# Kernel optimization log

Measured on AMD Instinct MI355X. Metric: run time of the kernel, lower is better.

Reference implementation:

```python
import jax, jax.numpy as jnp
import numpy as np

WS, OWS, NHEAD = 4, 6, 6          # window, overlap window = 4 + int(0.5*4), heads
B, CIN, COU, H, W = 2, 192, 192, 224, 224
MID = CIN  # r = 1


def calc_rpi_oca(ws=WS, ows=OWS):
    # relative position index between ws x ws query window and ows x ows overlapping kv window
    co = np.stack(np.meshgrid(np.arange(ws), np.arange(ws), indexing='ij')).reshape(2, -1)
    ce = np.stack(np.meshgrid(np.arange(ows), np.arange(ows), indexing='ij')).reshape(2, -1)
    rel = (ce[:, None, :] - co[:, :, None]).transpose(1, 2, 0) + (ws - 1)  # [ws*ws, ows*ows, 2], >= 0
    idx = rel[..., 0] * (ws + ows - 1) + rel[..., 1]                       # in [0, (ws+ows-1)^2)
    return jnp.asarray(idx)  # [16, 36]

RPI = calc_rpi_oca()


def conv2d(x, w, b, pad):
    out = jax.lax.conv_general_dilated(x, w, (1, 1), [(pad, pad), (pad, pad)],
                                       dimension_numbers=('NCHW', 'OIHW', 'NCHW'))
    return out + b[None, :, None, None]


def group_norm(x, g, b, groups, eps=1e-5):
    n = x.shape[0]
    xg = x.reshape(n, groups, -1)
    mu = xg.mean(-1, keepdims=True)
    var = xg.var(-1, keepdims=True)
    xn = ((xg - mu) * jax.lax.rsqrt(var + eps)).reshape(x.shape)
    return xn * g[None, :, None, None] + b[None, :, None, None]


def layer_norm(x, g, b, eps=1e-5):
    mu = x.mean(-1, keepdims=True)
    var = x.var(-1, keepdims=True)
    return (x - mu) * jax.lax.rsqrt(var + eps) * g + b


def ocab(x, h, w, ln1_g, ln1_b, qkv_w, qkv_b, rpb, proj_w, proj_b,
         ln2_g, ln2_b, fc1_w, fc1_b, fc2_w, fc2_b):
    b, _, c = x.shape
    nh, nw, d = h // WS, w // WS, c // NHEAD
    shortcut = x
    xn = layer_norm(x, ln1_g, ln1_b).reshape(b, h, w, c)
    qkv = xn @ qkv_w + qkv_b                                  # [b,h,w,3c] laid out [q|k|v]
    q = qkv[..., :c]
    kv = jnp.stack([qkv[..., c:2 * c], qkv[..., 2 * c:]])     # [2,b,h,w,c]
    # non-overlapping query windows -> [b*nwin, 16, NHEAD, d]
    qw = q.reshape(b, nh, WS, nw, WS, c).transpose(0, 1, 3, 2, 4, 5).reshape(b * nh * nw, WS * WS, NHEAD, d)
    # overlapping kv windows = Unfold(kernel=OWS, stride=WS, pad=(OWS-WS)//2)
    pad = (OWS - WS) // 2
    kvp = jnp.pad(kv, ((0, 0), (0, 0), (pad, pad), (pad, pad), (0, 0)))
    rows = (jnp.arange(nh) * WS)[:, None] + jnp.arange(OWS)[None, :]   # [nh, OWS]
    cols = (jnp.arange(nw) * WS)[:, None] + jnp.arange(OWS)[None, :]   # [nw, OWS]
    patches = kvp[:, :, rows[:, None, :, None], cols[None, :, None, :], :]  # [2,b,nh,nw,OWS,OWS,c]
    kvw = patches.reshape(2, b * nh * nw, OWS * OWS, NHEAD, d)
    kw, vw = kvw[0], kvw[1]
    attn = jnp.einsum('wqhd,wkhd->whqk', qw * (d ** -0.5), kw)  # [b*nwin, NHEAD, 16, 36]
    bias = rpb[RPI.reshape(-1)].reshape(WS * WS, OWS * OWS, NHEAD).transpose(2, 0, 1)
    attn = jax.nn.softmax(attn + bias[None], axis=-1)
    out = jnp.einsum('whqk,wkhd->wqhd', attn, vw).reshape(b, nh, nw, WS, WS, c)
    out = out.transpose(0, 1, 3, 2, 4, 5).reshape(b, h * w, c)  # window_reverse
    out = out @ proj_w + proj_b + shortcut
    xm = layer_norm(out, ln2_g, ln2_b)
    mlp = jax.nn.gelu(xm @ fc1_w + fc1_b, approximate=False) @ fc2_w + fc2_b
    return out + mlp


def atoca_forward(x, conv1_w, conv1_b, gn1_g, gn1_b, conv2_w, conv2_b, gn2_g, gn2_b,
                  conv3_w, conv3_b, ln1_g, ln1_b, qkv_w, qkv_b, rpb, proj_w, proj_b,
                  ln2_g, ln2_b, fc1_w, fc1_b, fc2_w, fc2_b):
    Bx, C, Hx, Wx = x.shape
    shortcut = x
    # raw row-major reshape, exactly as the torch code (not a spatial window partition)
    out = x.reshape(Bx * (Hx // WS) * (Wx // WS), C, WS, WS)
    out = conv2d(out, conv1_w, conv1_b, 1)
    out = jax.nn.silu(group_norm(out, gn1_g, gn1_b, NHEAD))
    out = out.transpose(0, 2, 3, 1).reshape(Bx, Hx * Wx, -1)
    out = ocab(out, Hx, Wx, ln1_g, ln1_b, qkv_w, qkv_b, rpb, proj_w, proj_b,
               ln2_g, ln2_b, fc1_w, fc1_b, fc2_w, fc2_b)
    out = out.reshape(Bx * (Hx // WS) * (Wx // WS), WS, WS, -1).transpose(0, 3, 1, 2)
    out = conv2d(out, conv2_w, conv2_b, 1)
    out = group_norm(out, gn2_g, gn2_b, NHEAD)
    out = out.reshape(Bx, -1, Hx, Wx)
    out = out + conv2d(shortcut, conv3_w, conv3_b, 0)
    return jax.nn.relu(out)


def setup_inputs() -> dict:
    key = jax.random.key(0)
    ks = iter(jax.random.split(key, 32))
    rn = lambda shape, s=0.02: (s * jax.random.normal(next(ks), shape)).astype(jnp.float32)
    return {
        'x': jax.random.normal(next(ks), (B, CIN, H, W), dtype=jnp.float32),
        'conv1_w': rn((MID, CIN, 3, 3)), 'conv1_b': rn((MID,)),
        'gn1_g': jnp.ones((MID,), jnp.float32), 'gn1_b': jnp.zeros((MID,), jnp.float32),
        'conv2_w': rn((COU, MID, 3, 3)), 'conv2_b': rn((COU,)),
        'gn2_g': jnp.ones((COU,), jnp.float32), 'gn2_b': jnp.zeros((COU,), jnp.float32),
        'conv3_w': rn((COU, CIN, 1, 1)), 'conv3_b': rn((COU,)),
        'ln1_g': jnp.ones((MID,), jnp.float32), 'ln1_b': jnp.zeros((MID,), jnp.float32),
        'qkv_w': rn((MID, 3 * MID)), 'qkv_b': rn((3 * MID,)),
        'rpb': rn(((WS + OWS - 1) ** 2, NHEAD)),
        'proj_w': rn((MID, MID)), 'proj_b': rn((MID,)),
        'ln2_g': jnp.ones((MID,), jnp.float32), 'ln2_b': jnp.zeros((MID,), jnp.float32),
        'fc1_w': rn((MID, 2 * MID)), 'fc1_b': rn((2 * MID,)),
        'fc2_w': rn((2 * MID, MID)), 'fc2_b': rn((MID,)),
    }


def reference(x, conv1_w, conv1_b, gn1_g, gn1_b, conv2_w, conv2_b, gn2_g, gn2_b,
              conv3_w, conv3_b, ln1_g, ln1_b, qkv_w, qkv_b, rpb, proj_w, proj_b,
              ln2_g, ln2_b, fc1_w, fc1_b, fc2_w, fc2_b):
    return atoca_forward(x, conv1_w, conv1_b, gn1_g, gn1_b, conv2_w, conv2_b, gn2_g, gn2_b,
                         conv3_w, conv3_b, ln1_g, ln1_b, qkv_w, qkv_b, rpb, proj_w, proj_b,
                         ln2_g, ln2_b, fc1_w, fc1_b, fc2_w, fc2_b)
```

## Files before the change

### kernel.cpp

```cpp
#include <hip/hip_runtime.h>
#include <hip/hip_bf16.h>
#include <math.h>

typedef __hip_bfloat16 bf16;
typedef __attribute__((ext_vector_type(8))) short s8v;
typedef __attribute__((ext_vector_type(4))) short s4v;
typedef __attribute__((ext_vector_type(4))) float f32x4;
typedef __attribute__((ext_vector_type(2))) _Float16 h2;

constexpr int CB   = 2;
constexpr int CH   = 224, CW = 224;
constexpr int NHW  = 56;
constexpr int NPATCH = CB * NHW * NHW;
constexpr int TOKPB  = CH * CW;
constexpr int MTOK   = CB * TOKPB;

constexpr size_t B_T0  = 0;
constexpr size_t B_P2  = B_T0 + 38535168;
constexpr size_t B_P3  = B_P2 + 115605504;
constexpr size_t B_P4  = B_P3 + 38535168;
constexpr size_t B_WF1 = B_P4 + 38535168;
constexpr size_t B_WF2 = B_WF1 + 1327104;
constexpr size_t B_W3F = B_WF2 + 1327104;
constexpr size_t B_WQ  = B_W3F + 147456;
constexpr size_t B_WP  = B_WQ + 221184;
constexpr size_t B_WG1 = B_WP + 73728;
constexpr size_t B_WG2 = B_WG1 + 147456;
constexpr size_t WS_NEEDED = B_WG2 + 147456;

__device__ __forceinline__ float ldf(const float* p) { return *p; }
__device__ __forceinline__ float ldf(const bf16* p)  { return __bfloat162float(*p); }
__device__ __forceinline__ void  stf(float* p, float v) { *p = v; }
__device__ __forceinline__ void  stf(bf16* p, float v)  { *p = __float2bfloat16(v); }
__device__ __forceinline__ unsigned short f2bf(float f) {
    unsigned u = __builtin_bit_cast(unsigned, f);
    unsigned r = (u + 0x7fffu + ((u >> 16) & 1u)) >> 16;
    return (unsigned short)r;
}
__device__ __forceinline__ float bf2f(short s) {
    unsigned u = ((unsigned)(unsigned short)s) << 16;
    return __builtin_bit_cast(float, u);
}

__global__ void build_wf_kernel(const float* __restrict__ w, short* __restrict__ wf) {
    int o = blockIdx.x * 256 + threadIdx.x;
    if (o >= 331776) return;
    int within = o & 511, frag = o >> 9;
    int l = within >> 3, j = within & 7;
    int nt = frag % 12, t2 = frag / 12, ks = t2 % 6, tap = t2 / 6;
    int co = nt * 16 + (l & 15);
    int ci = ks * 32 + (l >> 4) * 8 + j;
    wf[o] = (short)f2bf(w[(co * 192 + ci) * 9 + tap]);
}
__global__ void build_wgemm_kernel(const float* __restrict__ w, short* __restrict__ wf,
                                   int K, int N) {
    int o = blockIdx.x * 256 + threadIdx.x;
    if (o >= K * N) return;
    int j = o & 7, l = (o >> 3) & 63, f = o >> 9;
    int ntiles = N >> 4;
    int kt = f / ntiles, nt = f % ntiles;
    int k = kt * 32 + (l >> 4) * 8 + j;
    int col = nt * 16 + (l & 15);
    wf[o] = (short)f2bf(w[(size_t)k * N + col]);
}
__global__ void build_w3f_kernel(const float* __restrict__ w, short* __restrict__ wf) {
    int o = blockIdx.x * 256 + threadIdx.x;
    if (o >= 36864) return;
    int j = o & 7, l = (o >> 3) & 63, f = o >> 9;
    int kt = f / 12, ct = f % 12;
    int co = ct * 16 + (l & 15);
    int ci = kt * 32 + (l >> 4) * 8 + j;
    wf[o] = (short)f2bf(w[co * 192 + ci]);
}

template <bool FIRST>
__global__ __launch_bounds__(256, 4) void conv_mfma_kernel(
    const float* __restrict__ src, const short* __restrict__ wf,
    const float* __restrict__ bias, const float* __restrict__ gng,
    const float* __restrict__ gnb, bf16* __restrict__ dst)
{
    __shared__ short xs[13056];
    __shared__ float gsum[4][6], gsum2[4][6], gmu[4][6], grs[4][6];
    const int tid  = threadIdx.x;
    const int lane = tid & 63, wid = tid >> 6;
    const int n0   = blockIdx.x * 4;

    if (tid < 24) { gsum[tid / 6][tid % 6] = 0.f; gsum2[tid / 6][tid % 6] = 0.f; }
    for (int u = tid; u < 4 * 192; u += 256) {
        int q = u / 192;
        xs[q * 3264 + 3072 + (u % 192)] = 0;
    }

    const float4* sp = (const float4*)(src + (size_t)n0 * 3072);
    if (FIRST) {
        #pragma unroll
        for (int u = 0; u < 12; ++u) {
            int idx = u * 256 + tid;
            float4 v = sp[idx];
            int q = idx / 768;
            int li = (idx % 768) * 4;
            int ci = li >> 4, p0 = li & 15;
            float vv[4] = { v.x, v.y, v.z, v.w };
            #pragma unroll
            for (int k = 0; k < 4; ++k) {
                int row = p0 + k;
                int ba = q * 6528 + ((row * 384 + ci * 2) ^ ((row & 7) << 4));
                *(short*)((char*)xs + ba) = (short)f2bf(vv[k]);
            }
        }
    } else {
        #pragma unroll
        for (int u = 0; u < 12; ++u) {
            int idx = u * 256 + tid;
            float4 v = sp[idx];
            int r = idx / 48;
            int c0 = (idx % 48) * 4;
            int q = r >> 4, rl = r & 15;
            s4v pk = { (short)f2bf(v.x), (short)f2bf(v.y), (short)f2bf(v.z), (short)f2bf(v.w) };
            int ba = q * 6528 + ((rl * 384 + c0 * 2) ^ ((rl & 7) << 4));
            *(s4v*)((char*)xs + ba) = pk;
        }
    }
    __syncthreads();

    const int ntb = wid * 3;
    const int cl  = lane & 15;
    const int kg  = lane >> 4;
    f32x4 acc[3][4];
    #pragma unroll
    for (int t = 0; t < 3; ++t) {
        float bv = bias[(ntb + t) * 16 + cl];
        #pragma unroll
        for (int q = 0; q < 4; ++q) acc[t][q] = (f32x4){ bv, bv, bv, bv };
    }

    const int pi = cl >> 2, pj = cl & 3;
    const s8v* wf8 = (const s8v*)wf;

    for (int tap = 0; tap < 9; ++tap) {
        const int di = tap / 3, dj = tap % 3;
        const int ii = pi + di - 1, jj = pj + dj - 1;
        const bool valid = (ii >= 0 && ii < 4 && jj >= 0 && jj < 4);
        const int nr  = valid ? (ii * 4 + jj) : 16;
        const int rb  = nr * 384;
        const int swz = (nr & 7) << 4;
        #pragma unroll
        for (int ks = 0; ks < 6; ++ks) {
            const s8v* bp = wf8 + (size_t)((tap * 6 + ks) * 12) * 64 + lane;
            s8v b0 = bp[(ntb + 0) * 64];
            s8v b1 = bp[(ntb + 1) * 64];
            s8v b2 = bp[(ntb + 2) * 64];
            const int inner = (rb + ks * 64 + kg * 16) ^ swz;
            #pragma unroll
            for (int q = 0; q < 4; ++q) {
                s8v a = *(const s8v*)((const char*)xs + q * 6528 + inner);
                acc[0][q] = __builtin_amdgcn_mfma_f32_16x16x32_bf16(a, b0, acc[0][q], 0, 0, 0);
                acc[1][q] = __builtin_amdgcn_mfma_f32_16x16x32_bf16(a, b1, acc[1][q], 0, 0, 0);
                acc[2][q] = __builtin_amdgcn_mfma_f32_16x16x32_bf16(a, b2, acc[2][q], 0, 0, 0);
            }
        }
    }

    #pragma unroll
    for (int t = 0; t < 3; ++t) {
        const int g = (ntb + t) >> 1;
        #pragma unroll
        for (int q = 0; q < 4; ++q) {
            f32x4 A = acc[t][q];
            float s  = A[0] + A[1] + A[2] + A[3];
            float s2 = A[0]*A[0] + A[1]*A[1] + A[2]*A[2] + A[3]*A[3];
            #pragma unroll
            for (int off = 32; off; off >>= 1) { s += __shfl_xor(s, off); s2 += __shfl_xor(s2, off); }
            if (lane == 0) { atomicAdd(&gsum[q][g], s); atomicAdd(&gsum2[q][g], s2); }
        }
    }
    __syncthreads();
    if (tid < 24) {
        int q = tid / 6, g = tid % 6;
        float mu  = gsum[q][g] * (1.f / 512.f);
        float var = gsum2[q][g] * (1.f / 512.f) - mu * mu;
        gmu[q][g] = mu; grs[q][g] = rsqrtf(var + 1e-5f);
    }
    __syncthreads();

    if (FIRST) {
        #pragma unroll
        for (int t = 0; t < 3; ++t) {
            const int co = (ntb + t) * 16 + cl, g = (ntb + t) >> 1;
            const float gg = gng[co], gb = gnb[co];
            #pragma unroll
            for (int q = 0; q < 4; ++q) {
                const float mu = gmu[q][g], rs = grs[q][g];
                bf16* op = dst + (((size_t)(n0 + q) * 16) + kg * 4) * 192 + co;
                #pragma unroll
                for (int r = 0; r < 4; ++r) {
                    float v = (acc[t][q][r] - mu) * rs * gg + gb;
                    v = v / (1.f + expf(-v));
                    op[(size_t)r * 192] = __float2bfloat16(v);
                }
            }
        }
    } else {
        #pragma unroll
        for (int t = 0; t < 3; ++t) {
            const int co = (ntb + t) * 16 + cl, g = (ntb + t) >> 1;
            const float gg = gng[co], gb = gnb[co];
            #pragma unroll
            for (int q = 0; q < 4; ++q) {
                const float mu = gmu[q][g], rs = grs[q][g];
                #pragma unroll
                for (int r = 0; r < 4; ++r) {
                    float v = (acc[t][q][r] - mu) * rs * gg + gb;
                    xs[q * 3072 + co * 16 + kg * 4 + r] = (short)f2bf(v);
                }
            }
        }
        __syncthreads();
        s4v* dp = (s4v*)(dst + (size_t)n0 * 3072);
        const s4v* sps = (const s4v*)xs;
        #pragma unroll
        for (int u = 0; u < 12; ++u) {
            dp[u * 256 + tid] = sps[u * 256 + tid];
        }
    }
}

__global__ __launch_bounds__(256) void ln_kernel(
    const bf16* __restrict__ in, const float* __restrict__ g,
    const float* __restrict__ bb, bf16* __restrict__ out)
{
    const int row  = blockIdx.x * 4 + (threadIdx.x >> 6);
    const int lane = threadIdx.x & 63;
    const bf16* ip = in + (size_t)row * 192;
    float v0 = ldf(&ip[lane]), v1 = ldf(&ip[lane + 64]), v2 = ldf(&ip[lane + 128]);
    float s = v0 + v1 + v2, s2 = v0 * v0 + v1 * v1 + v2 * v2;
    #pragma unroll
    for (int off = 32; off; off >>= 1) { s += __shfl_xor(s, off); s2 += __shfl_xor(s2, off); }
    const float mu  = s * (1.f / 192.f);
    const float var = s2 * (1.f / 192.f) - mu * mu;
    const float rs  = rsqrtf(var + 1e-5f);
    bf16* op = out + (size_t)row * 192;
    stf(&op[lane],       (v0 - mu) * rs * g[lane]       + bb[lane]);
    stf(&op[lane + 64],  (v1 - mu) * rs * g[lane + 64]  + bb[lane + 64]);
    stf(&op[lane + 128], (v2 - mu) * rs * g[lane + 128] + bb[lane + 128]);
}

template <typename TO, bool RES, bool GELU_ACT>
__global__ __launch_bounds__(256) void gemm_mfma_kernel(
    const bf16* __restrict__ A, const short* __restrict__ wfb,
    const float* __restrict__ bias, const bf16* __restrict__ res,
    TO* __restrict__ out, int K, int N)
{
    const int tid = threadIdx.x, lane = tid & 63, wid = tid >> 6;
    const int m0 = blockIdx.x * 128, n0 = blockIdx.y * 64;
    const int cl = lane & 15, kg = lane >> 4;
    const int ntiles = N >> 4, nt0 = n0 >> 4;

    f32x4 acc[2][4];
    #pragma unroll
    for (int nf = 0; nf < 4; ++nf) {
        float bv = bias[n0 + nf * 16 + cl];
        acc[0][nf] = (f32x4){ bv, bv, bv, bv };
        acc[1][nf] = (f32x4){ bv, bv, bv, bv };
    }

    const s8v* wf8 = (const s8v*)wfb;
    const int nkt = K >> 5;
    for (int kt = 0; kt < nkt; ++kt) {
        s8v a0 = *(const s8v*)(A + (size_t)(m0 + wid * 32 +      cl) * K + kt * 32 + kg * 8);
        s8v a1 = *(const s8v*)(A + (size_t)(m0 + wid * 32 + 16 + cl) * K + kt * 32 + kg * 8);
        #pragma unroll
        for (int nf = 0; nf < 4; ++nf) {
            s8v b = wf8[(size_t)(kt * ntiles + nt0 + nf) * 64 + lane];
            acc[0][nf] = __builtin_amdgcn_mfma_f32_16x16x32_bf16(a0, b, acc[0][nf], 0, 0, 0);
            acc[1][nf] = __builtin_amdgcn_mfma_f32_16x16x32_bf16(a1, b, acc[1][nf], 0, 0, 0);
        }
    }

    #pragma unroll
    for (int rf = 0; rf < 2; ++rf) {
        #pragma unroll
        for (int nf = 0; nf < 4; ++nf) {
            const int col = n0 + nf * 16 + cl;
            #pragma unroll
            for (int r = 0; r < 4; ++r) {
                const int row = m0 + wid * 32 + rf * 16 + kg * 4 + r;
                float v = acc[rf][nf][r];
                if (GELU_ACT) v = 0.5f * v * (1.f + erff(v * 0.70710678118f));
                if (RES) v += ldf(&res[(size_t)row * N + col]);
                stf(&out[(size_t)row * N + col], v);
            }
        }
    }
}

constexpr int HSTR = 1160;
__global__ __launch_bounds__(128) void attn_kernel(
    const bf16* __restrict__ qkv, const float* __restrict__ rpb,
    bf16* __restrict__ out)
{
    __shared__ short kh[6 * HSTR];
    __shared__ short vh[6 * HSTR];
    const int w = blockIdx.x;
    const int b = w / (NHW * NHW), wi = w % (NHW * NHW);
    const int nhi = wi / NHW, nwi = wi % NHW;
    const int tid = threadIdx.x;
    const int r0 = nhi * 4 - 1, c0 = nwi * 4 - 1;

    #pragma unroll
    for (int it = 0; it < 14; ++it) {
        int v = tid + it * 128;
        if (v < 1728) {
            int h = v / 288, rem = v % 288, kj = rem >> 3, d0 = (rem & 7) * 4;
            int rr = r0 + kj / 6, cc = c0 + kj % 6;
            s4v kvk = { 0, 0, 0, 0 }, kvv = { 0, 0, 0, 0 };
            if (rr >= 0 && rr < CH && cc >= 0 && cc < CW) {
                size_t base = ((size_t)((b * CH + rr) * CW + cc)) * 576 + h * 32 + d0;
                kvk = *(const s4v*)(qkv + base + 192);
                kvv = *(const s4v*)(qkv + base + 384);
            }
            s4v ko, vo;
            #pragma unroll
            for (int e = 0; e < 4; ++e) {
                ko[e] = __builtin_bit_cast(short, (_Float16)bf2f(kvk[e]));
                vo[e] = __builtin_bit_cast(short, (_Float16)bf2f(kvv[e]));
            }
            int off = h * HSTR + kj * 32 + d0;
            *(s4v*)(kh + off) = ko;
            *(s4v*)(vh + off) = vo;
        }
    }
    __syncthreads();

    if (tid < 96) {
        const int h = tid >> 4, qi = tid & 15;
        const int qr = nhi * 4 + (qi >> 2), qc = nwi * 4 + (qi & 3);
        const bf16* qp = qkv + ((size_t)((b * CH + qr) * CW + qc)) * 576 + h * 32;
        h2 qh[16];
        #pragma unroll
        for (int u = 0; u < 4; ++u) {
            s8v qv = *(const s8v*)(qp + u * 8);
            #pragma unroll
            for (int e = 0; e < 4; ++e) {
                h2 p;
                p[0] = (_Float16)bf2f(qv[2 * e]);
                p[1] = (_Float16)bf2f(qv[2 * e + 1]);
                qh[u * 4 + e] = p;
            }
        }

        float sc[36];
        const char* khb = (const char*)(kh + h * HSTR);
        #pragma unroll
        for (int kj = 0; kj < 36; ++kj) {
            const uint4* kp = (const uint4*)(khb + kj * 64);
            uint4 k0 = kp[0], k1 = kp[1], k2 = kp[2], k3 = kp[3];
            unsigned kwv[16] = { k0.x, k0.y, k0.z, k0.w, k1.x, k1.y, k1.z, k1.w,
                                 k2.x, k2.y, k2.z, k2.w, k3.x, k3.y, k3.z, k3.w };
            float a = 0.f;
            #pragma unroll
            for (int e = 0; e < 16; ++e)
                a = __builtin_amdgcn_fdot2(__builtin_bit_cast(h2, kwv[e]), qh[e], a, false);
            const int rel0 = kj / 6 - (qi >> 2) + 3;
            const int rel1 = kj % 6 - (qi & 3) + 3;
            sc[kj] = a * 0.17677669529f + rpb[(rel0 * 9 + rel1) * 6 + h];
        }
        float mx = -1e30f;
        #pragma unroll
        for (int kj = 0; kj < 36; ++kj) mx = fmaxf(mx, sc[kj]);
        float sum = 0.f;
        #pragma unroll
        for (int kj = 0; kj < 36; ++kj) { sc[kj] = expf(sc[kj] - mx); sum += sc[kj]; }
        const float inv = 1.f / sum;

        float o[32];
        #pragma unroll
        for (int d = 0; d < 32; ++d) o[d] = 0.f;
        const char* vhb = (const char*)(vh + h * HSTR);
        #pragma unroll
        for (int kj = 0; kj < 36; ++kj) {
            const uint4* vp = (const uint4*)(vhb + kj * 64);
            uint4 v0 = vp[0], v1 = vp[1], v2 = vp[2], v3 = vp[3];
            unsigned vwv[16] = { v0.x, v0.y, v0.z, v0.w, v1.x, v1.y, v1.z, v1.w,
                                 v2.x, v2.y, v2.z, v2.w, v3.x, v3.y, v3.z, v3.w };
            const float p = sc[kj];
            #pragma unroll
            for (int e = 0; e < 16; ++e) {
                h2 hv = __builtin_bit_cast(h2, vwv[e]);
                o[2 * e]     += p * (float)hv[0];
                o[2 * e + 1] += p * (float)hv[1];
            }
        }
        bf16* op = out + ((size_t)(b * TOKPB + qr * CW + qc)) * 192 + h * 32;
        #pragma unroll
        for (int u = 0; u < 8; ++u) {
            s4v pk;
            #pragma unroll
            for (int e = 0; e < 4; ++e) pk[e] = (short)f2bf(o[u * 4 + e] * inv);
            *(s4v*)((bf16*)op + u * 4) = pk;
        }
    }
}

__global__ __launch_bounds__(256, 4) void final_mfma_kernel(
    const float* __restrict__ x, const short* __restrict__ w3f,
    const float* __restrict__ b3, const bf16* __restrict__ c2,
    float* __restrict__ out)
{
    __shared__ short xs2[12288];
    const int pix0 = blockIdx.x * 64;
    const int b    = blockIdx.y;
    const int tid = threadIdx.x, lane = tid & 63, wid = tid >> 6;
    const int cl = lane & 15, kg = lane >> 4;
    const float* xb = x + (size_t)b * (192 * TOKPB);

    #pragma unroll
    for (int u = 0; u < 12; ++u) {
        int idx = u * 256 + tid;
        int ci = idx >> 4, p4 = (idx & 15) << 2;
        float4 v = *(const float4*)(xb + (size_t)ci * TOKPB + pix0 + p4);
        float vv[4] = { v.x, v.y, v.z, v.w };
        #pragma unroll
        for (int k = 0; k < 4; ++k) {
            int row = p4 + k;
            int ba = (row * 384 + ci * 2) ^ ((row & 7) << 4);
            *(short*)((char*)xs2 + ba) = (short)f2bf(vv[k]);
        }
    }
    __syncthreads();

    const int ctb = wid * 3;
    f32x4 acc[3][4] = {};
    const s8v* wf8 = (const s8v*)w3f;

    #pragma unroll
    for (int kt = 0; kt < 6; ++kt) {
        s8v a0 = wf8[(size_t)(kt * 12 + ctb + 0) * 64 + lane];
        s8v a1 = wf8[(size_t)(kt * 12 + ctb + 1) * 64 + lane];
        s8v a2 = wf8[(size_t)(kt * 12 + ctb + 2) * 64 + lane];
        #pragma unroll
        for (int pt = 0; pt < 4; ++pt) {
            int row = pt * 16 + cl;
            int ba = (row * 384 + kt * 64 + kg * 16) ^ ((row & 7) << 4);
            s8v bfr = *(const s8v*)((const char*)xs2 + ba);
            acc[0][pt] = __builtin_amdgcn_mfma_f32_16x16x32_bf16(a0, bfr, acc[0][pt], 0, 0, 0);
            acc[1][pt] = __builtin_amdgcn_mfma_f32_16x16x32_bf16(a1, bfr, acc[1][pt], 0, 0, 0);
            acc[2][pt] = __builtin_amdgcn_mfma_f32_16x16x32_bf16(a2, bfr, acc[2][pt], 0, 0, 0);
        }
    }

    #pragma unroll
    for (int t = 0; t < 3; ++t) {
        #pragma unroll
        for (int r = 0; r < 4; ++r) {
            const int co = (ctb + t) * 16 + kg * 4 + r;
            const float bb = b3[co];
            const size_t rowbase = (size_t)b * (192 * TOKPB) + (size_t)co * TOKPB + pix0;
            #pragma unroll
            for (int pt = 0; pt < 4; ++pt) {
                const size_t f = rowbase + pt * 16 + cl;
                float v = acc[t][pt][r] + bb + bf2f(__builtin_bit_cast(short, c2[f]));
                out[f] = fmaxf(v, 0.f);
            }
        }
    }
}

extern "C" void kernel_launch(void* const* d_in, const int* in_sizes, int n_in,
                              void* d_out, int out_size, void* d_ws, size_t ws_size,
                              hipStream_t stream)
{
    if (ws_size < WS_NEEDED) return;

    const float* x       = (const float*)d_in[0];
    const float* conv1_w = (const float*)d_in[1];
    const float* conv1_b = (const float*)d_in[2];
    const float* gn1_g   = (const float*)d_in[3];
    const float* gn1_b   = (const float*)d_in[4];
    const float* conv2_w = (const float*)d_in[5];
    const float* conv2_b = (const float*)d_in[6];
    const float* gn2_g   = (const float*)d_in[7];
    const float* gn2_b   = (const float*)d_in[8];
    const float* conv3_w = (const float*)d_in[9];
    const float* conv3_b = (const float*)d_in[10];
    const float* ln1_g   = (const float*)d_in[11];
    const float* ln1_b   = (const float*)d_in[12];
    const float* qkv_w   = (const float*)d_in[13];
    const float* qkv_b   = (const float*)d_in[14];
    const float* rpb     = (const float*)d_in[15];
    const float* proj_w  = (const float*)d_in[16];
    const float* proj_b  = (const float*)d_in[17];
    const float* ln2_g   = (const float*)d_in[18];
    const float* ln2_b   = (const float*)d_in[19];
    const float* fc1_w   = (const float*)d_in[20];
    const float* fc1_b   = (const float*)d_in[21];
    const float* fc2_w   = (const float*)d_in[22];
    const float* fc2_b   = (const float*)d_in[23];

    char* wsb = (char*)d_ws;
    bf16*  T0  = (bf16*)(wsb + B_T0);
    bf16*  P2  = (bf16*)(wsb + B_P2);
    bf16*  P3  = (bf16*)(wsb + B_P3);
    bf16*  P4  = (bf16*)(wsb + B_P4);
    short* WF1 = (short*)(wsb + B_WF1);
    short* WF2 = (short*)(wsb + B_WF2);
    short* W3F = (short*)(wsb + B_W3F);
    short* WQ  = (short*)(wsb + B_WQ);
    short* WP  = (short*)(wsb + B_WP);
    short* WG1 = (short*)(wsb + B_WG1);
    short* WG2 = (short*)(wsb + B_WG2);
    float* OUT = (float*)d_out;

    build_wf_kernel<<<(331776 + 255) / 256, 256, 0, stream>>>(conv1_w, WF1);
    build_wf_kernel<<<(331776 + 255) / 256, 256, 0, stream>>>(conv2_w, WF2);
    build_w3f_kernel<<<(36864 + 255) / 256, 256, 0, stream>>>(conv3_w, W3F);
    build_wgemm_kernel<<<(110592 + 255) / 256, 256, 0, stream>>>(qkv_w, WQ, 192, 576);
    build_wgemm_kernel<<<(36864 + 255) / 256, 256, 0, stream>>>(proj_w, WP, 192, 192);
    build_wgemm_kernel<<<(73728 + 255) / 256, 256, 0, stream>>>(fc1_w, WG1, 192, 384);
    build_wgemm_kernel<<<(73728 + 255) / 256, 256, 0, stream>>>(fc2_w, WG2, 384, 192);

    conv_mfma_kernel<true><<<NPATCH / 4, 256, 0, stream>>>(x, WF1, conv1_b, gn1_g, gn1_b, T0);
    ln_kernel<<<MTOK / 4, 256, 0, stream>>>(T0, ln1_g, ln1_b, P3);
    gemm_mfma_kernel<bf16, false, false><<<dim3(MTOK / 128, 9), 256, 0, stream>>>(P3, WQ, qkv_b, nullptr, P2, 192, 576);
    attn_kernel<<<NPATCH, 128, 0, stream>>>(P2, rpb, P3);
    gemm_mfma_kernel<bf16, true, false><<<dim3(MTOK / 128, 3), 256, 0, stream>>>(P3, WP, proj_b, T0, P4, 192, 192);
    ln_kernel<<<MTOK / 4, 256, 0, stream>>>(P4, ln2_g, ln2_b, P3);
    gemm_mfma_kernel<bf16, false, true><<<dim3(MTOK / 128, 6), 256, 0, stream>>>(P3, WG1, fc1_b, nullptr, P2, 192, 384);
    gemm_mfma_kernel<float, true, false><<<dim3(MTOK / 128, 3), 256, 0, stream>>>(P2, WG2, fc2_b, P4, OUT, 384, 192);
    conv_mfma_kernel<false><<<NPATCH / 4, 256, 0, stream>>>(OUT, WF2, conv2_b, gn2_g, gn2_b, P4);
    final_mfma_kernel<<<dim3(TOKPB / 64, CB), 256, 0, stream>>>(x, W3F, conv3_b, P4, OUT);
}
```

Before: 623.5 us.

## Fuse LayerNorm into QKV/FC1 GEMMs, bf16 MLP output, and read V directly

Removes both standalone LayerNorm kernels and folds the normalization into the A-operand load of the QKV and FC1 GEMMs, which recompute per-row statistics for every N tile. The FC2 output now goes to a bf16 buffer instead of fp32, and the second conv reads bf16 directly, which cuts traffic in both kernels. Attention no longer stages V through shared memory and reads it straight from global memory as bf16. Since each N-tile block redoes the LN arithmetic, there is extra compute in the GEMMs. The direct V reads rely on cache hits across the overlapping windows.

```diff
diff --git a/kernel.cpp b/kernel.cpp
--- a/kernel.cpp
+++ b/kernel.cpp
@@ -75,7 +75,7 @@
 
 template <bool FIRST>
 __global__ __launch_bounds__(256, 4) void conv_mfma_kernel(
-    const float* __restrict__ src, const short* __restrict__ wf,
+    const void* __restrict__ srcv, const short* __restrict__ wf,
     const float* __restrict__ bias, const float* __restrict__ gng,
     const float* __restrict__ gnb, bf16* __restrict__ dst)
 {
@@ -91,8 +91,8 @@
         xs[q * 3264 + 3072 + (u % 192)] = 0;
     }
 
-    const float4* sp = (const float4*)(src + (size_t)n0 * 3072);
-    if (FIRST) {
+    if constexpr (FIRST) {
+        const float4* sp = (const float4*)((const float*)srcv + (size_t)n0 * 3072);
         #pragma unroll
         for (int u = 0; u < 12; ++u) {
             int idx = u * 256 + tid;
@@ -109,16 +109,15 @@
             }
         }
     } else {
-        #pragma unroll
-        for (int u = 0; u < 12; ++u) {
-            int idx = u * 256 + tid;
-            float4 v = sp[idx];
-            int r = idx / 48;
-            int c0 = (idx % 48) * 4;
+        const s8v* sp8 = (const s8v*)((const bf16*)srcv + (size_t)n0 * 3072);
+        #pragma unroll
+        for (int u = 0; u < 6; ++u) {
+            int li = u * 256 + tid;
+            int r = li / 24, ch = li % 24;
             int q = r >> 4, rl = r & 15;
-            s4v pk = { (short)f2bf(v.x), (short)f2bf(v.y), (short)f2bf(v.z), (short)f2bf(v.w) };
-            int ba = q * 6528 + ((rl * 384 + c0 * 2) ^ ((rl & 7) << 4));
-            *(s4v*)((char*)xs + ba) = pk;
+            s8v val = sp8[li];
+            int ba = q * 6528 + ((rl * 384 + ch * 16) ^ ((rl & 7) << 4));
+            *(s8v*)((char*)xs + ba) = val;
         }
     }
     __syncthreads();
@@ -183,7 +182,7 @@
     }
     __syncthreads();
 
-    if (FIRST) {
+    if constexpr (FIRST) {
         #pragma unroll
         for (int t = 0; t < 3; ++t) {
             const int co = (ntb + t) * 16 + cl, g = (ntb + t) >> 1;
@@ -225,31 +224,12 @@
     }
 }
 
-__global__ __launch_bounds__(256) void ln_kernel(
-    const bf16* __restrict__ in, const float* __restrict__ g,
-    const float* __restrict__ bb, bf16* __restrict__ out)
-{
-    const int row  = blockIdx.x * 4 + (threadIdx.x >> 6);
-    const int lane = threadIdx.x & 63;
-    const bf16* ip = in + (size_t)row * 192;
-    float v0 = ldf(&ip[lane]), v1 = ldf(&ip[lane + 64]), v2 = ldf(&ip[lane + 128]);
-    float s = v0 + v1 + v2, s2 = v0 * v0 + v1 * v1 + v2 * v2;
-    #pragma unroll
-    for (int off = 32; off; off >>= 1) { s += __shfl_xor(s, off); s2 += __shfl_xor(s2, off); }
-    const float mu  = s * (1.f / 192.f);
-    const float var = s2 * (1.f / 192.f) - mu * mu;
-    const float rs  = rsqrtf(var + 1e-5f);
-    bf16* op = out + (size_t)row * 192;
-    stf(&op[lane],       (v0 - mu) * rs * g[lane]       + bb[lane]);
-    stf(&op[lane + 64],  (v1 - mu) * rs * g[lane + 64]  + bb[lane + 64]);
-    stf(&op[lane + 128], (v2 - mu) * rs * g[lane + 128] + bb[lane + 128]);
-}
-
-template <typename TO, bool RES, bool GELU_ACT>
+template <typename TO, bool RES, bool GELU_ACT, bool LN>
 __global__ __launch_bounds__(256) void gemm_mfma_kernel(
     const bf16* __restrict__ A, const short* __restrict__ wfb,
     const float* __restrict__ bias, const bf16* __restrict__ res,
-    TO* __restrict__ out, int K, int N)
+    TO* __restrict__ out, int K, int N,
+    const float* __restrict__ lng, const float* __restrict__ lnb)
 {
     const int tid = threadIdx.x, lane = tid & 63, wid = tid >> 6;
     const int m0 = blockIdx.x * 128, n0 = blockIdx.y * 64;
@@ -265,15 +245,60 @@
     }
 
     const s8v* wf8 = (const s8v*)wfb;
-    const int nkt = K >> 5;
-    for (int kt = 0; kt < nkt; ++kt) {
-        s8v a0 = *(const s8v*)(A + (size_t)(m0 + wid * 32 +      cl) * K + kt * 32 + kg * 8);
-        s8v a1 = *(const s8v*)(A + (size_t)(m0 + wid * 32 + 16 + cl) * K + kt * 32 + kg * 8);
-        #pragma unroll
-        for (int nf = 0; nf < 4; ++nf) {
-            s8v b = wf8[(size_t)(kt * ntiles + nt0 + nf) * 64 + lane];
-            acc[0][nf] = __builtin_amdgcn_mfma_f32_16x16x32_bf16(a0, b, acc[0][nf], 0, 0, 0);
-            acc[1][nf] = __builtin_amdgcn_mfma_f32_16x16x32_bf16(a1, b, acc[1][nf], 0, 0, 0);
+
+    if constexpr (LN) {
+        s8v af[2][6];
+        const int r0 = m0 + wid * 32 + cl;
+        #pragma unroll
+        for (int kt = 0; kt < 6; ++kt) {
+            af[0][kt] = *(const s8v*)(A + (size_t)r0 * 192 + kt * 32 + kg * 8);
+            af[1][kt] = *(const s8v*)(A + (size_t)(r0 + 16) * 192 + kt * 32 + kg * 8);
+        }
+        #pragma unroll
+        for (int r = 0; r < 2; ++r) {
+            float s = 0.f, s2 = 0.f;
+            #pragma unroll
+            for (int kt = 0; kt < 6; ++kt)
+                #pragma unroll
+                for (int j = 0; j < 8; ++j) {
+                    float v = bf2f(af[r][kt][j]);
+                    s += v; s2 += v * v;
+                }
+            s  += __shfl_xor(s, 16);  s2 += __shfl_xor(s2, 16);
+            s  += __shfl_xor(s, 32);  s2 += __shfl_xor(s2, 32);
+            const float mu = s * (1.f / 192.f);
+            const float rs = rsqrtf(s2 * (1.f / 192.f) - mu * mu + 1e-5f);
+            #pragma unroll
+            for (int kt = 0; kt < 6; ++kt) {
+                const float* gp = lng + kt * 32 + kg * 8;
+                const float* bp = lnb + kt * 32 + kg * 8;
+                #pragma unroll
+                for (int j = 0; j < 8; ++j) {
+                    float v = (bf2f(af[r][kt][j]) - mu) * rs * gp[j] + bp[j];
+                    af[r][kt][j] = (short)f2bf(v);
+                }
+            }
+        }
+        #pragma unroll
+        for (int kt = 0; kt < 6; ++kt) {
+            #pragma unroll
+            for (int nf = 0; nf < 4; ++nf) {
+                s8v b = wf8[(size_t)(kt * ntiles + nt0 + nf) * 64 + lane];
+                acc[0][nf] = __builtin_amdgcn_mfma_f32_16x16x32_bf16(af[0][kt], b, acc[0][nf], 0, 0, 0);
+                acc[1][nf] = __builtin_amdgcn_mfma_f32_16x16x32_bf16(af[1][kt], b, acc[1][nf], 0, 0, 0);
+            }
+        }
+    } else {
+        const int nkt = K >> 5;
+        for (int kt = 0; kt < nkt; ++kt) {
+            s8v a0 = *(const s8v*)(A + (size_t)(m0 + wid * 32 +      cl) * K + kt * 32 + kg * 8);
+            s8v a1 = *(const s8v*)(A + (size_t)(m0 + wid * 32 + 16 + cl) * K + kt * 32 + kg * 8);
+            #pragma unroll
+            for (int nf = 0; nf < 4; ++nf) {
+                s8v b = wf8[(size_t)(kt * ntiles + nt0 + nf) * 64 + lane];
+                acc[0][nf] = __builtin_amdgcn_mfma_f32_16x16x32_bf16(a0, b, acc[0][nf], 0, 0, 0);
+                acc[1][nf] = __builtin_amdgcn_mfma_f32_16x16x32_bf16(a1, b, acc[1][nf], 0, 0, 0);
+            }
         }
     }
 
@@ -300,7 +325,6 @@
     bf16* __restrict__ out)
 {
     __shared__ short kh[6 * HSTR];
-    __shared__ short vh[6 * HSTR];
     const int w = blockIdx.x;
     const int b = w / (NHW * NHW), wi = w % (NHW * NHW);
     const int nhi = wi / NHW, nwi = wi % NHW;
@@ -308,26 +332,21 @@
     const int r0 = nhi * 4 - 1, c0 = nwi * 4 - 1;
 
     #pragma unroll
-    for (int it = 0; it < 14; ++it) {
+    for (int it = 0; it < 7; ++it) {
         int v = tid + it * 128;
-        if (v < 1728) {
-            int h = v / 288, rem = v % 288, kj = rem >> 3, d0 = (rem & 7) * 4;
+        if (v < 864) {
+            int h = v / 144, rem = v % 144, kj = rem >> 2, d0 = (rem & 3) * 8;
             int rr = r0 + kj / 6, cc = c0 + kj % 6;
-            s4v kvk = { 0, 0, 0, 0 }, kvv = { 0, 0, 0, 0 };
+            s8v kvk = { 0, 0, 0, 0, 0, 0, 0, 0 };
             if (rr >= 0 && rr < CH && cc >= 0 && cc < CW) {
                 size_t base = ((size_t)((b * CH + rr) * CW + cc)) * 576 + h * 32 + d0;
-                kvk = *(const s4v*)(qkv + base + 192);
-                kvv = *(const s4v*)(qkv + base + 384);
-            }
-            s4v ko, vo;
-            #pragma unroll
-            for (int e = 0; e < 4; ++e) {
+                kvk = *(const s8v*)(qkv + base + 192);
+            }
+            s8v ko;
+            #pragma unroll
+            for (int e = 0; e < 8; ++e)
                 ko[e] = __builtin_bit_cast(short, (_Float16)bf2f(kvk[e]));
-                vo[e] = __builtin_bit_cast(short, (_Float16)bf2f(kvv[e]));
-            }
-            int off = h * HSTR + kj * 32 + d0;
-            *(s4v*)(kh + off) = ko;
-            *(s4v*)(vh + off) = vo;
+            *(s8v*)(kh + h * HSTR + kj * 32 + d0) = ko;
         }
     }
     __syncthreads();
@@ -376,19 +395,21 @@
         float o[32];
         #pragma unroll
         for (int d = 0; d < 32; ++d) o[d] = 0.f;
-        const char* vhb = (const char*)(vh + h * HSTR);
         #pragma unroll
         for (int kj = 0; kj < 36; ++kj) {
-            const uint4* vp = (const uint4*)(vhb + kj * 64);
+            const int rr = r0 + kj / 6, cc = c0 + kj % 6;
+            if (rr < 0 || rr >= CH || cc < 0 || cc >= CW) continue;
+            const uint4* vp = (const uint4*)(qkv + ((size_t)((b * CH + rr) * CW + cc)) * 576 + 384 + h * 32);
             uint4 v0 = vp[0], v1 = vp[1], v2 = vp[2], v3 = vp[3];
             unsigned vwv[16] = { v0.x, v0.y, v0.z, v0.w, v1.x, v1.y, v1.z, v1.w,
                                  v2.x, v2.y, v2.z, v2.w, v3.x, v3.y, v3.z, v3.w };
             const float p = sc[kj];
             #pragma unroll
             for (int e = 0; e < 16; ++e) {
-                h2 hv = __builtin_bit_cast(h2, vwv[e]);
-                o[2 * e]     += p * (float)hv[0];
-                o[2 * e + 1] += p * (float)hv[1];
+                float lo = __builtin_bit_cast(float, vwv[e] << 16);
+                float hi = __builtin_bit_cast(float, vwv[e] & 0xffff0000u);
+                o[2 * e]     += p * lo;
+                o[2 * e + 1] += p * hi;
             }
         }
         bf16* op = out + ((size_t)(b * TOKPB + qr * CW + qc)) * 192 + h * 32;
@@ -520,13 +541,15 @@
     build_wgemm_kernel<<<(73728 + 255) / 256, 256, 0, stream>>>(fc2_w, WG2, 384, 192);
 
     conv_mfma_kernel<true><<<NPATCH / 4, 256, 0, stream>>>(x, WF1, conv1_b, gn1_g, gn1_b, T0);
-    ln_kernel<<<MTOK / 4, 256, 0, stream>>>(T0, ln1_g, ln1_b, P3);
-    gemm_mfma_kernel<bf16, false, false><<<dim3(MTOK / 128, 9), 256, 0, stream>>>(P3, WQ, qkv_b, nullptr, P2, 192, 576);
+    gemm_mfma_kernel<bf16, false, false, true><<<dim3(MTOK / 128, 9), 256, 0, stream>>>(
+        T0, WQ, qkv_b, nullptr, P2, 192, 576, ln1_g, ln1_b);
     attn_kernel<<<NPATCH, 128, 0, stream>>>(P2, rpb, P3);
-    gemm_mfma_kernel<bf16, true, false><<<dim3(MTOK / 128, 3), 256, 0, stream>>>(P3, WP, proj_b, T0, P4, 192, 192);
-    ln_kernel<<<MTOK / 4, 256, 0, stream>>>(P4, ln2_g, ln2_b, P3);
-    gemm_mfma_kernel<bf16, false, true><<<dim3(MTOK / 128, 6), 256, 0, stream>>>(P3, WG1, fc1_b, nullptr, P2, 192, 384);
-    gemm_mfma_kernel<float, true, false><<<dim3(MTOK / 128, 3), 256, 0, stream>>>(P2, WG2, fc2_b, P4, OUT, 384, 192);
-    conv_mfma_kernel<false><<<NPATCH / 4, 256, 0, stream>>>(OUT, WF2, conv2_b, gn2_g, gn2_b, P4);
+    gemm_mfma_kernel<bf16, true, false, false><<<dim3(MTOK / 128, 3), 256, 0, stream>>>(
+        P3, WP, proj_b, T0, P4, 192, 192, nullptr, nullptr);
+    gemm_mfma_kernel<bf16, false, true, true><<<dim3(MTOK / 128, 6), 256, 0, stream>>>(
+        P4, WG1, fc1_b, nullptr, P2, 192, 384, ln2_g, ln2_b);
+    gemm_mfma_kernel<bf16, true, false, false><<<dim3(MTOK / 128, 3), 256, 0, stream>>>(
+        P2, WG2, fc2_b, P4, P3, 384, 192, nullptr, nullptr);
+    conv_mfma_kernel<false><<<NPATCH / 4, 256, 0, stream>>>(P3, WF2, conv2_b, gn2_g, gn2_b, P4);
     final_mfma_kernel<<<dim3(TOKPB / 64, CB), 256, 0, stream>>>(x, W3F, conv3_b, P4, OUT);
 }
```

After: 620.1 us. About the same (-0.6%).
